# Optimization experiments

Hardware: AMD Instinct MI355X
Metric: run time of the kernel (lower is better)

## Reference

```python
import jax, jax.numpy as jnp
import numpy as np

DILATIONS = [1, 2, 4, 8, 16, 32, 64, 128, 256, 512] * 2
WD = 128   # residual/gate channels
SD = 512   # skip channels
VOCAB = 256
FIELD = int(np.sum(DILATIONS)) + 2  # receptive field = 2048


def setup_inputs() -> dict:
    key = jax.random.key(0)
    ks = jax.random.split(key, 10)
    B, T = 4, 16384
    L = len(DILATIONS)
    y = jax.random.randint(ks[0], (B, T), 0, VOCAB)
    embed = jax.random.normal(ks[1], (VOCAB, WD), dtype=jnp.float32) * 0.1
    # dilated causal conv: kernel_size=2, wd -> 2*wd (gate stacking)
    Wd = jax.random.normal(ks[2], (L, 2 * WD, WD, 2), dtype=jnp.float32) * 0.05
    bd = jnp.zeros((L, 2 * WD), dtype=jnp.float32)
    # skip 1x1 conv: wd -> sd
    Ws = jax.random.normal(ks[3], (L, SD, WD, 1), dtype=jnp.float32) * 0.05
    bs = jnp.zeros((L, SD), dtype=jnp.float32)
    # residual 1x1 conv: wd -> wd
    Wr = jax.random.normal(ks[4], (L, WD, WD, 1), dtype=jnp.float32) * 0.05
    br = jnp.zeros((L, WD), dtype=jnp.float32)
    # post convs (bias=False)
    W1 = jax.random.normal(ks[5], (SD, SD, 1), dtype=jnp.float32) * 0.05
    W2 = jax.random.normal(ks[6], (VOCAB, SD, 1), dtype=jnp.float32) * 0.05
    return {"y": y, "embed": embed, "Wd": Wd, "bd": bd, "Ws": Ws,
            "bs": bs, "Wr": Wr, "br": br, "W1": W1, "W2": W2}


def reference(y, embed, Wd, bd, Ws, bs, Wr, br, W1, W2):
    # embedding -> [B, C, T]
    x = jnp.transpose(embed[y], (0, 2, 1))
    finalout = x.shape[2] - (FIELD - 1)
    skip = None
    for i, d in enumerate(DILATIONS):
        # dilated valid conv with kernel size 2 == two shifted 1x1 matmuls
        in_act = (jnp.einsum('oc,bct->bot', Wd[i, :, :, 0], x[:, :, :-d]) +
                  jnp.einsum('oc,bct->bot', Wd[i, :, :, 1], x[:, :, d:]) +
                  bd[i][None, :, None])                       # [B, 2*WD, T-d]
        acts = jnp.tanh(in_act[:, :WD]) * jax.nn.sigmoid(in_act[:, WD:])
        res = jnp.einsum('oc,bct->bot', Wr[i, :, :, 0], acts) + br[i][None, :, None]
        sk = (jnp.einsum('oc,bct->bot', Ws[i, :, :, 0], acts[:, :, -finalout:]) +
              bs[i][None, :, None])                            # [B, SD, finalout]
        skip = sk if skip is None else skip + sk
        x = res + x[:, :, d:]
    out = jax.nn.relu(skip)
    out = jax.nn.relu(jnp.einsum('oc,bct->bot', W1[:, :, 0], out))
    out = jnp.einsum('oc,bct->bot', W2[:, :, 0], out)          # [B, 256, finalout]
    return out
```

## Files before the change

kernel.cpp:

```cpp
#include <hip/hip_runtime.h>
#include <cstddef>

#define B_    4
#define T_    16384
#define FOUT_ 14337
#define FOUTP 14464
#define NL_   20
#define XSTR  ((size_t)T_*128)
#define ABSTR ((size_t)FOUTP*128)
#define ALSTR ((size_t)B_*FOUTP*128)
#define SBSTR ((size_t)FOUTP*512)

typedef float    f32x16 __attribute__((ext_vector_type(16)));
typedef _Float16 f16x8  __attribute__((ext_vector_type(8)));

__device__ _Float16 g_xh0[(size_t)B_*T_*128];
__device__ _Float16 g_xh1[(size_t)B_*T_*128];
__device__ _Float16 g_WdF0[(size_t)NL_*256*128];
__device__ _Float16 g_WdF1[(size_t)NL_*256*128];
__device__ _Float16 g_WrF [(size_t)NL_*128*128];
__device__ _Float16 g_WsF [(size_t)512*2560];
__device__ _Float16 g_W1F [(size_t)512*512];
__device__ _Float16 g_W2F [(size_t)256*512];
__device__ float    g_bssum[512];
__device__ _Float16 g_acts[(size_t)NL_*B_*FOUTP*128];
__device__ _Float16 g_skipF[(size_t)B_*FOUTP*512];
__device__ _Float16 g_h1F [(size_t)B_*FOUTP*512];

__device__ __forceinline__ float sigm_(float x){ return 1.0f/(1.0f+__expf(-x)); }
__device__ __forceinline__ float tanh_(float x){ return 1.0f - 2.0f/(__expf(2.0f*x)+1.0f); }
__device__ __forceinline__ f32x16 MFMA32(f16x8 a, f16x8 b, f32x16 c){
  return __builtin_amdgcn_mfma_f32_32x32x16_f16(a, b, c, 0, 0, 0);
}

typedef const __attribute__((address_space(1))) _Float16 gash;
typedef __attribute__((address_space(3))) _Float16 lash;
__device__ __forceinline__ void gld_lds16(const _Float16* g, _Float16* l){
  __builtin_amdgcn_global_load_lds((gash*)g, (lash*)l, 16, 0, 0);
}

__global__ void cvt_wd(const float* __restrict__ Wd){
  int i = blockIdx.x*256 + threadIdx.x;
  if (i >= NL_*256*16) return;
  int row = i >> 4, koct = i & 15;
  const float* s = Wd + ((size_t)row*128 + koct*8)*2;
  int lane = (koct&1)*32 + (row&31);
  size_t addr = (size_t)((row>>5)*8 + (koct>>1))*512 + lane*8;
  union { _Float16 h[8]; uint4 v; } u0, u1;
#pragma unroll
  for (int j=0;j<8;j++){ u0.h[j]=(_Float16)s[2*j]; u1.h[j]=(_Float16)s[2*j+1]; }
  *(uint4*)((void*)(g_WdF0 + addr)) = u0.v;
  *(uint4*)((void*)(g_WdF1 + addr)) = u1.v;
}
__global__ void cvt_rm(const float* __restrict__ src, int which, int M, int K){
  int i = blockIdx.x*256 + threadIdx.x;
  if (i >= M*(K>>3)) return;
  int row = i / (K>>3), koct = i % (K>>3);
  const float* s = src + (size_t)row*K + koct*8;
  int lane = (koct&1)*32 + (row&31);
  size_t addr = ((size_t)(row>>5)*(K>>4) + (koct>>1))*512 + lane*8;
  union { _Float16 h[8]; uint4 v; } u;
#pragma unroll
  for (int j=0;j<8;j++) u.h[j]=(_Float16)s[j];
  _Float16* dst = (which==0)?g_WrF:(which==1)?g_W1F:g_W2F;
  *(uint4*)((void*)(dst + addr)) = u.v;
}
__global__ void cvt_ws(const float* __restrict__ Ws){
  int i = blockIdx.x*256 + threadIdx.x;
  if (i >= NL_*512*16) return;
  int l = i >> 13, o = (i>>4)&511, coct = i&15;
  const float* s = Ws + ((size_t)(l*512+o))*128 + coct*8;
  int lane = (coct&1)*32 + (o&31);
  size_t addr = ((size_t)(o>>5)*160 + (size_t)(l*8 + (coct>>1)))*512 + lane*8;
  union { _Float16 h[8]; uint4 v; } u;
#pragma unroll
  for (int j=0;j<8;j++) u.h[j]=(_Float16)s[j];
  *(uint4*)((void*)(g_WsF + addr)) = u.v;
}
__global__ void bssum_k(const float* __restrict__ bs){
  int o = threadIdx.x;
  float s = 0.f;
  for (int l=0;l<NL_;l++) s += bs[l*512 + o];
  g_bssum[o] = s;
}

__global__ void embed_kernel(const int* __restrict__ y, const float* __restrict__ embed){
  int gid = blockIdx.x*256 + threadIdx.x;
  int bt = gid >> 4, c8 = gid & 15;
  if (bt < B_*T_){
    int idx = y[bt];
    const float* e = embed + (size_t)idx*128 + c8*8;
    union { _Float16 h[8]; uint4 v; } u;
#pragma unroll
    for (int j=0;j<8;j++) u.h[j]=(_Float16)e[j];
    *(uint4*)((void*)(g_xh0 + (size_t)bt*128 + c8*8)) = u.v;
  }
}

__global__ __launch_bounds__(256,3) void layer16(
    int swap, int l, int d, int Tout, int ss,
    const float* __restrict__ bd_l, const float* __restrict__ br_l)
{
  const _Float16* __restrict__ xin  = swap ? g_xh1 : g_xh0;
  _Float16* __restrict__       xout = swap ? g_xh0 : g_xh1;

  __shared__ _Float16 X0s[16*520];
  __shared__ _Float16 X1s[16*520];
  __shared__ _Float16 ACs[16*520];

  const int tid = threadIdx.x;
  const int w   = tid >> 6;
  const int lane= tid & 63;
  const int ln2 = lane & 31;
  const int h   = lane >> 5;
  const int b   = blockIdx.y;
  const int t0  = blockIdx.x*64;
  const int ntv = min(64, Tout - t0);
  const int limit = Tout + d - 1;
  const _Float16* __restrict__ xb = xin + (size_t)b*XSTR;

#pragma unroll
  for (int it=0; it<4; it++){
    int t = (tid>>4) + it*16, c16 = tid&15;
    int s0 = t0 + t;     if (s0 > limit) s0 = limit;
    int s1 = t0 + t + d; if (s1 > limit) s1 = limit;
    *(uint4*)((void*)&X0s[c16*520 + t*8]) = *(const uint4*)((const void*)(xb + (size_t)s0*128 + c16*8));
    *(uint4*)((void*)&X1s[c16*520 + t*8]) = *(const uint4*)((const void*)(xb + (size_t)s1*128 + c16*8));
  }
  __syncthreads();

  f32x16 aB[2][2];
#pragma unroll
  for (int mi=0;mi<2;mi++)
#pragma unroll
    for (int nt=0;nt<2;nt++)
#pragma unroll
      for (int r=0;r<16;r++) aB[mi][nt][r] = 0.f;

#pragma unroll
  for (int tap=0; tap<2; tap++){
    const _Float16* __restrict__ Xs = tap ? X1s : X0s;
    const _Float16* __restrict__ Wt = (tap ? g_WdF1 : g_WdF0) + (size_t)l*32768;
    const _Float16* aT = Wt + (size_t)w*4096 + lane*8;
    const _Float16* aS = Wt + (size_t)(4+w)*4096 + lane*8;
#pragma unroll
    for (int ks=0; ks<8; ks++){
      f16x8 bfr[2];
#pragma unroll
      for (int nt=0; nt<2; nt++)
        bfr[nt] = *(const f16x8*)((const void*)&Xs[(ks*2+h)*520 + (nt*32+ln2)*8]);
      f16x8 fT = *(const f16x8*)((const void*)(aT + ks*512));
      f16x8 fS = *(const f16x8*)((const void*)(aS + ks*512));
#pragma unroll
      for (int nt=0; nt<2; nt++){
        aB[0][nt] = MFMA32(fT, bfr[nt], aB[0][nt]);
        aB[1][nt] = MFMA32(fS, bfr[nt], aB[1][nt]);
      }
    }
  }

#pragma unroll
  for (int nt=0; nt<2; nt++)
#pragma unroll
    for (int rq=0; rq<4; rq++){
      int c0 = w*32 + rq*8 + 4*h;
      union { _Float16 hh[4]; ushort4 v; } pk;
#pragma unroll
      for (int rr=0; rr<4; rr++){
        float it_ = aB[0][nt][rq*4+rr] + bd_l[c0+rr];
        float is_ = aB[1][nt][rq*4+rr] + bd_l[128+c0+rr];
        pk.hh[rr] = (_Float16)(tanh_(it_)*sigm_(is_));
      }
      *(ushort4*)((void*)&ACs[(w*4+rq)*520 + (nt*32+ln2)*8 + 4*h]) = pk.v;
    }
  __syncthreads();

  f32x16 aC[2];
#pragma unroll
  for (int nt=0;nt<2;nt++)
#pragma unroll
    for (int r=0;r<16;r++) aC[nt][r] = 0.f;
  {
    const _Float16* aW = g_WrF + (size_t)l*16384 + (size_t)w*4096 + lane*8;
#pragma unroll
    for (int ks=0; ks<8; ks++){
      f16x8 bfr[2];
#pragma unroll
      for (int nt=0; nt<2; nt++)
        bfr[nt] = *(const f16x8*)((const void*)&ACs[(ks*2+h)*520 + (nt*32+ln2)*8]);
      f16x8 fW = *(const f16x8*)((const void*)(aW + ks*512));
#pragma unroll
      for (int nt=0; nt<2; nt++)
        aC[nt] = MFMA32(fW, bfr[nt], aC[nt]);
    }
  }

#pragma unroll
  for (int nt=0; nt<2; nt++){
    int t = nt*32 + ln2;
    if (t < ntv){
      size_t xrow = (size_t)b*XSTR + (size_t)(t0+t)*128;
#pragma unroll
      for (int rq=0; rq<4; rq++){
        int c0 = w*32 + rq*8 + 4*h;
        union { ushort4 v; _Float16 hh[4]; } xr;
        xr.v = *(const ushort4*)((const void*)&X1s[(w*4+rq)*520 + t*8 + 4*h]);
        union { _Float16 hh[4]; ushort4 v; } ov;
#pragma unroll
        for (int rr=0; rr<4; rr++)
          ov.hh[rr] = (_Float16)(aC[nt][rq*4+rr] + br_l[c0+rr] + (float)xr.hh[rr]);
        *(ushort4*)((void*)(xout + xrow + c0)) = ov.v;
      }
    }
  }

  _Float16* __restrict__ actsB = g_acts + (size_t)l*ALSTR + (size_t)b*ABSTR;
#pragma unroll
  for (int it=0; it<4; it++){
    int t = (tid>>4) + it*16, c16 = tid&15;
    int ts = t0 + t - ss;
    if (t < ntv && ts >= 0 && ts < FOUT_){
      size_t addr = (size_t)(ts>>5)*4096 + (size_t)(c16>>1)*512 + ((c16&1)*32 + (ts&31))*8;
      *(uint4*)((void*)(actsB + addr)) = *(const uint4*)((const void*)&ACs[c16*520 + t*8]);
    }
  }
}

template<int MODE>
__global__ __launch_bounds__(512,4) void gemm_stream(float* __restrict__ outF){
  constexpr int NSTEP = (MODE==0)?160:32;
  constexpr int NSC   = NSTEP/4;
  const _Float16* __restrict__ A    = (MODE==0)?g_WsF:(MODE==1)?g_W1F:g_W2F;
  const _Float16* __restrict__ Bsrc = (MODE==0)?g_acts:(MODE==1)?g_skipF:g_h1F;

  __shared__ __align__(16) _Float16 Bs[4][8192];

  const int tid = threadIdx.x;
  const int w   = tid >> 6;
  const int lane= tid & 63;
  const int ln2 = lane & 31;
  const int h   = lane >> 5;

  int lin = blockIdx.x;
  int mhalf, pairIdx;
  if (MODE==2){ mhalf = 0; pairIdx = lin; }
  else {
    mhalf   = (lin>>3)&1;
    pairIdx = ((lin>>4)<<3) | (lin&7);
    if (pairIdx >= 452) return;
  }
  const int b    = pairIdx / 113;
  const int tsb  = pairIdx - b*113;
  const int ts0  = tsb*128;
  const int mtile= mhalf*8 + w;

  const _Float16* Gq[2];
#pragma unroll
  for (int q=0;q<2;q++){
    int nt = (w*2+q)&3;
    size_t tile = (size_t)tsb*4 + nt;
    Gq[q] = (MODE==0) ? (Bsrc + (size_t)b*ABSTR + tile*4096  + lane*8)
                      : (Bsrc + (size_t)b*SBSTR + tile*16384 + lane*8);
  }

  const _Float16* Aw = A + (size_t)mtile*((size_t)NSTEP*512) + lane*8;

  f32x16 acc[4];
#pragma unroll
  for (int nt=0;nt<4;nt++)
#pragma unroll
    for (int r=0;r<16;r++) acc[nt][r] = 0.f;

  auto STAGE = [&](int buf, int sc){
#pragma unroll
    for (int q=0;q<2;q++){
      int bi   = w*2 + q;
      int kslq = bi>>2;
      const _Float16* g;
      if (MODE==0){
        int ks = sc*4 + kslq;
        g = Gq[q] + (size_t)(ks>>3)*ALSTR + (size_t)(ks&7)*512;
      } else {
        g = Gq[q] + (size_t)(sc*4 + kslq)*512;
      }
      gld_lds16(g, &Bs[buf][(size_t)bi*512]);
    }
  };

  STAGE(0,0);
  STAGE(1,1);
  asm volatile("s_waitcnt vmcnt(2)" ::: "memory");
  __builtin_amdgcn_sched_barrier(0);
  __builtin_amdgcn_s_barrier();

  for (int c=0; c<NSC; ++c){
    const int buf = c & 3;
    f16x8 af[4];
#pragma unroll
    for (int j=0;j<4;j++)
      af[j] = *(const f16x8*)((const void*)(Aw + (size_t)(c*4+j)*512));
    __builtin_amdgcn_sched_barrier(0);
    if (c+2 < NSC) STAGE((c+2)&3, c+2);
    __builtin_amdgcn_sched_barrier(0);
#pragma unroll
    for (int j=0;j<4;j++){
      f16x8 bfr[4];
#pragma unroll
      for (int nt=0;nt<4;nt++)
        bfr[nt] = *(const f16x8*)((const void*)&Bs[buf][(size_t)(j*4+nt)*512 + lane*8]);
#pragma unroll
      for (int nt=0;nt<4;nt++)
        acc[nt] = MFMA32(af[j], bfr[nt], acc[nt]);
    }
    __builtin_amdgcn_sched_barrier(0);
    __builtin_amdgcn_s_barrier();
  }

  if (MODE != 2){
    _Float16* __restrict__ dstb = ((MODE==0)?g_skipF:g_h1F) + (size_t)b*SBSTR;
#pragma unroll
    for (int nt=0; nt<4; nt++){
      int ts = ts0 + nt*32 + ln2;
      if (ts >= FOUT_) continue;
#pragma unroll
      for (int rq=0; rq<4; rq++){
        int m0 = mtile*32 + rq*8 + 4*h;
        union { _Float16 hh[4]; ushort4 v; } pk;
#pragma unroll
        for (int rr=0; rr<4; rr++){
          float vv = acc[nt][rq*4+rr];
          if (MODE==0) vv += g_bssum[m0+rr];
          pk.hh[rr] = (_Float16)fmaxf(vv, 0.f);
        }
        size_t addr = (size_t)(ts>>5)*16384 + (size_t)(mtile*2 + (rq>>1))*512
                    + ((rq&1)*32 + (ts&31))*8 + 4*h;
        *(ushort4*)((void*)(dstb + addr)) = pk.v;
      }
    }
  } else {
#pragma unroll
    for (int nt=0; nt<4; nt++){
      int ts = ts0 + nt*32 + ln2;
      if (ts >= FOUT_) continue;
#pragma unroll
      for (int rq=0; rq<4; rq++){
        int m0 = w*32 + rq*8 + 4*h;
#pragma unroll
        for (int rr=0; rr<4; rr++)
          outF[((size_t)(b*256 + m0 + rr))*FOUT_ + ts] = acc[nt][rq*4+rr];
      }
    }
  }
}

extern "C" void kernel_launch(void* const* d_in, const int* in_sizes, int n_in,
                              void* d_out, int out_size, void* d_ws, size_t ws_size,
                              hipStream_t stream) {
  const int*   y     = (const int*)  d_in[0];
  const float* embed = (const float*)d_in[1];
  const float* Wd    = (const float*)d_in[2];
  const float* bd    = (const float*)d_in[3];
  const float* Ws    = (const float*)d_in[4];
  const float* bs    = (const float*)d_in[5];
  const float* Wr    = (const float*)d_in[6];
  const float* br    = (const float*)d_in[7];
  const float* W1    = (const float*)d_in[8];
  const float* W2    = (const float*)d_in[9];
  float* out = (float*)d_out;
  (void)d_ws; (void)ws_size;

  cvt_wd<<<dim3(320), dim3(256), 0, stream>>>(Wd);
  cvt_rm<<<dim3(160), dim3(256), 0, stream>>>(Wr, 0, NL_*128, 128);
  cvt_rm<<<dim3(128), dim3(256), 0, stream>>>(W1, 1, 512, 512);
  cvt_rm<<<dim3( 64), dim3(256), 0, stream>>>(W2, 2, 256, 512);
  cvt_ws<<<dim3(640), dim3(256), 0, stream>>>(Ws);
  bssum_k<<<dim3(1), dim3(512), 0, stream>>>(bs);

  embed_kernel<<<dim3((B_*T_*16)/256), dim3(256), 0, stream>>>(y, embed);

  static const int DIL[NL_] = {1,2,4,8,16,32,64,128,256,512,
                               1,2,4,8,16,32,64,128,256,512};
  int swap = 0;
  int Tin = T_;
  for (int i=0;i<NL_;i++){
    int d = DIL[i];
    int Tout = Tin - d;
    dim3 grid((Tout+63)/64, B_);
    layer16<<<grid, dim3(256), 0, stream>>>(
        swap, i, d, Tout, Tout - FOUT_, bd + (size_t)i*256, br + (size_t)i*128);
    swap ^= 1;
    Tin = Tout;
  }

  gemm_stream<0><<<dim3(928), dim3(512), 0, stream>>>(nullptr);
  gemm_stream<1><<<dim3(928), dim3(512), 0, stream>>>(nullptr);
  gemm_stream<2><<<dim3(452), dim3(512), 0, stream>>>(out);
}
```

Baseline: 924.1 us.

## Process two time tiles per layer block with register prefetch of next tile

Each layer block now handles two 64-step time tiles. It issues global loads for the second tile into registers while the first tile's MFMA work runs, then writes them to shared memory after a barrier. The grid is halved to match. The skip-stream GEMM also raises wave priority around its MFMA section with s_setprio. The intent is to hide global load latency and cut block launch overhead, at the cost of extra registers, fewer blocks and more barriers.

```diff
diff --git a/kernel.cpp b/kernel.cpp
--- a/kernel.cpp
+++ b/kernel.cpp
@@ -114,116 +114,147 @@
   const int ln2 = lane & 31;
   const int h   = lane >> 5;
   const int b   = blockIdx.y;
-  const int t0  = blockIdx.x*64;
-  const int ntv = min(64, Tout - t0);
   const int limit = Tout + d - 1;
   const _Float16* __restrict__ xb = xin + (size_t)b*XSTR;
-
-#pragma unroll
-  for (int it=0; it<4; it++){
-    int t = (tid>>4) + it*16, c16 = tid&15;
-    int s0 = t0 + t;     if (s0 > limit) s0 = limit;
-    int s1 = t0 + t + d; if (s1 > limit) s1 = limit;
-    *(uint4*)((void*)&X0s[c16*520 + t*8]) = *(const uint4*)((const void*)(xb + (size_t)s0*128 + c16*8));
-    *(uint4*)((void*)&X1s[c16*520 + t*8]) = *(const uint4*)((const void*)(xb + (size_t)s1*128 + c16*8));
-  }
+  const int st_t0 = tid>>4, st_c16 = tid&15;
+  const int tbase = blockIdx.x*128;
+
+  uint4 p0[4], p1[4];
+#define LOADP(T0)                                                              \
+  {                                                                            \
+    _Pragma("unroll")                                                          \
+    for (int it=0; it<4; it++){                                                \
+      int t = st_t0 + it*16;                                                   \
+      int s0 = (T0) + t;     if (s0 > limit) s0 = limit;                       \
+      int s1 = (T0) + t + d; if (s1 > limit) s1 = limit;                       \
+      p0[it] = *(const uint4*)((const void*)(xb + (size_t)s0*128 + st_c16*8)); \
+      p1[it] = *(const uint4*)((const void*)(xb + (size_t)s1*128 + st_c16*8)); \
+    }                                                                          \
+  }
+#define WRITEP()                                                               \
+  {                                                                            \
+    _Pragma("unroll")                                                          \
+    for (int it=0; it<4; it++){                                                \
+      int t = st_t0 + it*16;                                                   \
+      *(uint4*)((void*)&X0s[st_c16*520 + t*8]) = p0[it];                       \
+      *(uint4*)((void*)&X1s[st_c16*520 + t*8]) = p1[it];                       \
+    }                                                                          \
+  }
+
+  LOADP(tbase);
+  WRITEP();
   __syncthreads();
 
-  f32x16 aB[2][2];
-#pragma unroll
-  for (int mi=0;mi<2;mi++)
-#pragma unroll
-    for (int nt=0;nt<2;nt++)
-#pragma unroll
-      for (int r=0;r<16;r++) aB[mi][nt][r] = 0.f;
-
-#pragma unroll
-  for (int tap=0; tap<2; tap++){
-    const _Float16* __restrict__ Xs = tap ? X1s : X0s;
-    const _Float16* __restrict__ Wt = (tap ? g_WdF1 : g_WdF0) + (size_t)l*32768;
-    const _Float16* aT = Wt + (size_t)w*4096 + lane*8;
-    const _Float16* aS = Wt + (size_t)(4+w)*4096 + lane*8;
-#pragma unroll
-    for (int ks=0; ks<8; ks++){
-      f16x8 bfr[2];
+  for (int ti=0; ti<2; ++ti){
+    const int t0 = tbase + ti*64;
+    if (ti==0) LOADP(tbase+64);
+    if (t0 < Tout){
+      const int ntv = min(64, Tout - t0);
+
+      f32x16 aB[2][2];
+#pragma unroll
+      for (int mi=0;mi<2;mi++)
+#pragma unroll
+        for (int nt=0;nt<2;nt++)
+#pragma unroll
+          for (int r=0;r<16;r++) aB[mi][nt][r] = 0.f;
+
+#pragma unroll
+      for (int tap=0; tap<2; tap++){
+        const _Float16* __restrict__ Xs = tap ? X1s : X0s;
+        const _Float16* __restrict__ Wt = (tap ? g_WdF1 : g_WdF0) + (size_t)l*32768;
+        const _Float16* aT = Wt + (size_t)w*4096 + lane*8;
+        const _Float16* aS = Wt + (size_t)(4+w)*4096 + lane*8;
+#pragma unroll
+        for (int ks=0; ks<8; ks++){
+          f16x8 bfr[2];
+#pragma unroll
+          for (int nt=0; nt<2; nt++)
+            bfr[nt] = *(const f16x8*)((const void*)&Xs[(ks*2+h)*520 + (nt*32+ln2)*8]);
+          f16x8 fT = *(const f16x8*)((const void*)(aT + ks*512));
+          f16x8 fS = *(const f16x8*)((const void*)(aS + ks*512));
+#pragma unroll
+          for (int nt=0; nt<2; nt++){
+            aB[0][nt] = MFMA32(fT, bfr[nt], aB[0][nt]);
+            aB[1][nt] = MFMA32(fS, bfr[nt], aB[1][nt]);
+          }
+        }
+      }
+
 #pragma unroll
       for (int nt=0; nt<2; nt++)
-        bfr[nt] = *(const f16x8*)((const void*)&Xs[(ks*2+h)*520 + (nt*32+ln2)*8]);
-      f16x8 fT = *(const f16x8*)((const void*)(aT + ks*512));
-      f16x8 fS = *(const f16x8*)((const void*)(aS + ks*512));
+#pragma unroll
+        for (int rq=0; rq<4; rq++){
+          int c0 = w*32 + rq*8 + 4*h;
+          union { _Float16 hh[4]; ushort4 v; } pk;
+#pragma unroll
+          for (int rr=0; rr<4; rr++){
+            float it_ = aB[0][nt][rq*4+rr] + bd_l[c0+rr];
+            float is_ = aB[1][nt][rq*4+rr] + bd_l[128+c0+rr];
+            pk.hh[rr] = (_Float16)(tanh_(it_)*sigm_(is_));
+          }
+          *(ushort4*)((void*)&ACs[(w*4+rq)*520 + (nt*32+ln2)*8 + 4*h]) = pk.v;
+        }
+      __syncthreads();
+
+      f32x16 aC[2];
+#pragma unroll
+      for (int nt=0;nt<2;nt++)
+#pragma unroll
+        for (int r=0;r<16;r++) aC[nt][r] = 0.f;
+      {
+        const _Float16* aW = g_WrF + (size_t)l*16384 + (size_t)w*4096 + lane*8;
+#pragma unroll
+        for (int ks=0; ks<8; ks++){
+          f16x8 bfr[2];
+#pragma unroll
+          for (int nt=0; nt<2; nt++)
+            bfr[nt] = *(const f16x8*)((const void*)&ACs[(ks*2+h)*520 + (nt*32+ln2)*8]);
+          f16x8 fW = *(const f16x8*)((const void*)(aW + ks*512));
+#pragma unroll
+          for (int nt=0; nt<2; nt++)
+            aC[nt] = MFMA32(fW, bfr[nt], aC[nt]);
+        }
+      }
+
 #pragma unroll
       for (int nt=0; nt<2; nt++){
-        aB[0][nt] = MFMA32(fT, bfr[nt], aB[0][nt]);
-        aB[1][nt] = MFMA32(fS, bfr[nt], aB[1][nt]);
-      }
-    }
-  }
-
-#pragma unroll
-  for (int nt=0; nt<2; nt++)
-#pragma unroll
-    for (int rq=0; rq<4; rq++){
-      int c0 = w*32 + rq*8 + 4*h;
-      union { _Float16 hh[4]; ushort4 v; } pk;
-#pragma unroll
-      for (int rr=0; rr<4; rr++){
-        float it_ = aB[0][nt][rq*4+rr] + bd_l[c0+rr];
-        float is_ = aB[1][nt][rq*4+rr] + bd_l[128+c0+rr];
-        pk.hh[rr] = (_Float16)(tanh_(it_)*sigm_(is_));
-      }
-      *(ushort4*)((void*)&ACs[(w*4+rq)*520 + (nt*32+ln2)*8 + 4*h]) = pk.v;
-    }
-  __syncthreads();
-
-  f32x16 aC[2];
-#pragma unroll
-  for (int nt=0;nt<2;nt++)
-#pragma unroll
-    for (int r=0;r<16;r++) aC[nt][r] = 0.f;
-  {
-    const _Float16* aW = g_WrF + (size_t)l*16384 + (size_t)w*4096 + lane*8;
-#pragma unroll
-    for (int ks=0; ks<8; ks++){
-      f16x8 bfr[2];
-#pragma unroll
-      for (int nt=0; nt<2; nt++)
-        bfr[nt] = *(const f16x8*)((const void*)&ACs[(ks*2+h)*520 + (nt*32+ln2)*8]);
-      f16x8 fW = *(const f16x8*)((const void*)(aW + ks*512));
-#pragma unroll
-      for (int nt=0; nt<2; nt++)
-        aC[nt] = MFMA32(fW, bfr[nt], aC[nt]);
-    }
-  }
-
-#pragma unroll
-  for (int nt=0; nt<2; nt++){
-    int t = nt*32 + ln2;
-    if (t < ntv){
-      size_t xrow = (size_t)b*XSTR + (size_t)(t0+t)*128;
-#pragma unroll
-      for (int rq=0; rq<4; rq++){
-        int c0 = w*32 + rq*8 + 4*h;
-        union { ushort4 v; _Float16 hh[4]; } xr;
-        xr.v = *(const ushort4*)((const void*)&X1s[(w*4+rq)*520 + t*8 + 4*h]);
-        union { _Float16 hh[4]; ushort4 v; } ov;
-#pragma unroll
-        for (int rr=0; rr<4; rr++)
-          ov.hh[rr] = (_Float16)(aC[nt][rq*4+rr] + br_l[c0+rr] + (float)xr.hh[rr]);
-        *(ushort4*)((void*)(xout + xrow + c0)) = ov.v;
-      }
-    }
-  }
-
-  _Float16* __restrict__ actsB = g_acts + (size_t)l*ALSTR + (size_t)b*ABSTR;
-#pragma unroll
-  for (int it=0; it<4; it++){
-    int t = (tid>>4) + it*16, c16 = tid&15;
-    int ts = t0 + t - ss;
-    if (t < ntv && ts >= 0 && ts < FOUT_){
-      size_t addr = (size_t)(ts>>5)*4096 + (size_t)(c16>>1)*512 + ((c16&1)*32 + (ts&31))*8;
-      *(uint4*)((void*)(actsB + addr)) = *(const uint4*)((const void*)&ACs[c16*520 + t*8]);
-    }
-  }
+        int t = nt*32 + ln2;
+        if (t < ntv){
+          size_t xrow = (size_t)b*XSTR + (size_t)(t0+t)*128;
+#pragma unroll
+          for (int rq=0; rq<4; rq++){
+            int c0 = w*32 + rq*8 + 4*h;
+            union { ushort4 v; _Float16 hh[4]; } xr;
+            xr.v = *(const ushort4*)((const void*)&X1s[(w*4+rq)*520 + t*8 + 4*h]);
+            union { _Float16 hh[4]; ushort4 v; } ov;
+#pragma unroll
+            for (int rr=0; rr<4; rr++)
+              ov.hh[rr] = (_Float16)(aC[nt][rq*4+rr] + br_l[c0+rr] + (float)xr.hh[rr]);
+            *(ushort4*)((void*)(xout + xrow + c0)) = ov.v;
+          }
+        }
+      }
+
+      _Float16* __restrict__ actsB = g_acts + (size_t)l*ALSTR + (size_t)b*ABSTR;
+#pragma unroll
+      for (int it=0; it<4; it++){
+        int t = st_t0 + it*16, c16 = st_c16;
+        int ts = t0 + t - ss;
+        if (t < ntv && ts >= 0 && ts < FOUT_){
+          size_t addr = (size_t)(ts>>5)*4096 + (size_t)(c16>>1)*512 + ((c16&1)*32 + (ts&31))*8;
+          *(uint4*)((void*)(actsB + addr)) = *(const uint4*)((const void*)&ACs[c16*520 + t*8]);
+        }
+      }
+    }
+    if (ti==0){
+      __syncthreads();
+      WRITEP();
+      __syncthreads();
+    }
+  }
+#undef LOADP
+#undef WRITEP
 }
 
 template<int MODE>
@@ -302,6 +333,7 @@
     __builtin_amdgcn_sched_barrier(0);
     if (c+2 < NSC) STAGE((c+2)&3, c+2);
     __builtin_amdgcn_sched_barrier(0);
+    __builtin_amdgcn_s_setprio(1);
 #pragma unroll
     for (int j=0;j<4;j++){
       f16x8 bfr[4];
@@ -312,6 +344,7 @@
       for (int nt=0;nt<4;nt++)
         acc[nt] = MFMA32(af[j], bfr[nt], acc[nt]);
     }
+    __builtin_amdgcn_s_setprio(0);
     __builtin_amdgcn_sched_barrier(0);
     __builtin_amdgcn_s_barrier();
   }
@@ -385,7 +418,7 @@
   for (int i=0;i<NL_;i++){
     int d = DIL[i];
     int Tout = Tin - d;
-    dim3 grid((Tout+63)/64, B_);
+    dim3 grid((Tout+127)/128, B_);
     layer16<<<grid, dim3(256), 0, stream>>>(
         swap, i, d, Tout, Tout - FOUT_, bd + (size_t)i*256, br + (size_t)i*128);
     swap ^= 1;
```

Result: slower. 1.263 ms (+36.6%).
